# Kernel optimization log

Measured on AMD Instinct MI355X. Metric: run time of the kernel, lower is better.

Reference implementation:

```python
import jax, jax.numpy as jnp
import numpy as np

D = 768; NH = 12; DH = 64; DEPTH = 12; P = 16; IMG = 224; NC = 1000; DFF = 3072
GAMMA = 0.01; MIN_TOKENS = 16; EPS = 1e-6
SCALE = DH ** -0.5
NPATCH = (IMG // P) ** 2  # 196


def _ln(x, w, b, eps=1e-6):
    mu = x.mean(-1, keepdims=True)
    var = ((x - mu) ** 2).mean(-1, keepdims=True)
    return (x - mu) * jax.lax.rsqrt(var + eps) * w + b


def _block(x, p):
    # one pre-norm ViT block; returns new x, attention matrix A [B,H,T,T], values v [B,H,T,DH]
    (l1w, l1b, qw, qb, pw, pb, l2w, l2b, f1w, f1b, f2w, f2b) = p
    B, T, _ = x.shape
    qkv = _ln(x, l1w, l1b) @ qw + qb                      # [B,T,3D]
    qkv = qkv.reshape(B, T, 3, NH, DH).transpose(2, 0, 3, 1, 4)
    q, k, v = qkv[0], qkv[1], qkv[2]                      # [B,H,T,DH]
    A = jax.nn.softmax(jnp.einsum('bhtd,bhsd->bhts', q, k) * SCALE, axis=-1)
    out = jnp.einsum('bhts,bhsd->bhtd', A, v).transpose(0, 2, 1, 3).reshape(B, T, NH * DH)
    x = x + out @ pw + pb
    h = jax.nn.gelu(_ln(x, l2w, l2b) @ f1w + f1b, approximate=False)
    x = x + h @ f2w + f2b
    return x, A, v


def _embed(x, patch_w, patch_b, cls_token, pos_embed):
    B = x.shape[0]
    feat = jax.lax.conv_general_dilated(x, patch_w, (P, P), 'VALID',
                                        dimension_numbers=('NCHW', 'OIHW', 'NCHW'))  # [B,D,14,14]
    feat = feat.reshape(B, D, -1).transpose(0, 2, 1) + patch_b                       # [B,196,D]
    cls = jnp.broadcast_to(cls_token, (B, 1, D))
    return jnp.concatenate([cls, feat], axis=1) + pos_embed                          # [B,197,D]


def setup_inputs() -> dict:
    key = jax.random.key(0)
    ks = jax.random.split(key, 12)
    s = 0.02
    n = lambda k, shape: jax.random.normal(k, shape, jnp.float32) * s
    return {
        'x': jax.random.normal(ks[0], (32, 3, IMG, IMG), jnp.float32),
        'patch_w': n(ks[1], (D, 3, P, P)),
        'patch_b': jnp.zeros((D,), jnp.float32),
        'cls_token': n(ks[2], (1, 1, D)),
        'pos_embed': n(ks[3], (1, NPATCH + 1, D)),
        'ln1_w': jnp.ones((DEPTH, D), jnp.float32),
        'ln1_b': jnp.zeros((DEPTH, D), jnp.float32),
        'qkv_w': n(ks[4], (DEPTH, D, 3 * D)),
        'qkv_b': jnp.zeros((DEPTH, 3 * D), jnp.float32),
        'proj_w': n(ks[5], (DEPTH, D, D)),
        'proj_b': jnp.zeros((DEPTH, D), jnp.float32),
        'ln2_w': jnp.ones((DEPTH, D), jnp.float32),
        'ln2_b': jnp.zeros((DEPTH, D), jnp.float32),
        'fc1_w': n(ks[6], (DEPTH, D, DFF)),
        'fc1_b': jnp.zeros((DEPTH, DFF), jnp.float32),
        'fc2_w': n(ks[7], (DEPTH, DFF, D)),
        'fc2_b': jnp.zeros((DEPTH, D), jnp.float32),
        'norm_w': jnp.ones((D,), jnp.float32),
        'norm_b': jnp.zeros((D,), jnp.float32),
        'head_w': n(ks[8], (D, NC)),
        'head_b': jnp.zeros((NC,), jnp.float32),
    }


def reference(x, patch_w, patch_b, cls_token, pos_embed, ln1_w, ln1_b, qkv_w, qkv_b,
              proj_w, proj_b, ln2_w, ln2_b, fc1_w, fc1_b, fc2_w, fc2_b,
              norm_w, norm_b, head_w, head_b):
    # NOTE: token pruning produces data-dependent shapes, so this runs eagerly
    # (Python control flow on concrete values), exactly mirroring the torch code.
    x = _embed(x, patch_w, patch_b, cls_token, pos_embed)
    N = x.shape[1] - 1
    prev_mass = None
    for l in range(DEPTH):
        p = (ln1_w[l], ln1_b[l], qkv_w[l], qkv_b[l], proj_w[l], proj_b[l],
             ln2_w[l], ln2_b[l], fc1_w[l], fc1_b[l], fc2_w[l], fc2_b[l])
        x, A, v = _block(x, p)
        if N <= MIN_TOKENS:
            continue
        Am = A.mean(axis=1)                                   # [B,T,T] head-mean attention
        Vm = v.mean(axis=1)                                   # [B,T,DH] head-mean values
        rho = (1.0 + Am[:, 0, 0] * jnp.linalg.norm(Vm[:, 0], axis=-1)).mean()
        A_cls = Am[:, 0, 1:N + 1]                             # [B,N] cls->patch attention
        V_pt = Vm[:, 1:N + 1]
        Vc = V_pt - V_pt.mean(axis=1, keepdims=True)
        Vn = jnp.linalg.norm(Vc, axis=-1)                     # [B,N]
        mu = Vn.mean(axis=1, keepdims=True)
        sd = Vn.std(axis=1, keepdims=True, ddof=1)            # torch.std is unbiased
        J = A_cls * jax.nn.relu((Vn - mu) / (sd + EPS))       # [B,N] Jacobian score
        mass = J.sum(axis=1).mean()
        if prev_mass is not None:
            eta = mass / (prev_mass + EPS)
            keep_ratio = jnp.clip(rho * eta, 0.25, 4.0) ** (-GAMMA)
            N_next = max(MIN_TOKENS, int(N * float(keep_ratio)))
        else:
            N_next = N
        if N_next < N:
            idx = jnp.sort(jax.lax.top_k(J.mean(axis=0), N_next)[1]) + 1
            keep = jnp.concatenate([jnp.zeros((1,), idx.dtype), idx])
            x = x[:, keep]
            N = N_next
        prev_mass = mass
    x = _ln(x, norm_w, norm_b)
    return x[:, 0] @ head_w + head_b
```

## Files before the change

### kernel.cpp

```cpp
#include <hip/hip_runtime.h>
#include <math.h>

#define D 768
#define NH 12
#define DH 64
#define DEPTH 12
#define TMAX 197
#define NPATCH 196
#define BATCH 32
#define DFF 3072
#define NC 1000
#define QSTRIDE 2304
#define SCALE 0.125f
#define EPSF 1e-6f
#define MPAD 6400

typedef __bf16 bf16x8 __attribute__((ext_vector_type(8)));
typedef float f32x4 __attribute__((ext_vector_type(4)));
typedef short sshort8 __attribute__((ext_vector_type(8)));


__device__ __forceinline__ short f2bf(float x) {
  unsigned u = __float_as_uint(x);
  u = u + 0x7fffu + ((u >> 16) & 1u);
  return (short)(u >> 16);
}
__device__ __forceinline__ float bf2f(short h) {
  return __uint_as_float(((unsigned)(unsigned short)h) << 16);
}
__device__ __forceinline__ void bsplit(float x, short* hp, short* lp) {
  short h = f2bf(x);
  *hp = h;
  *lp = f2bf(x - bf2f(h));
}

__device__ __forceinline__ void gll16(const void* g, void* l) {
  __builtin_amdgcn_global_load_lds(
      (const __attribute__((address_space(1))) void*)g,
      (__attribute__((address_space(3))) void*)l, 16, 0, 0);
}


__device__ __forceinline__ float block_reduce_sum(float v, float* red, int tid) {
  red[tid] = v; __syncthreads();
  #pragma unroll
  for (int o = 128; o > 0; o >>= 1) { if (tid < o) red[tid] += red[tid + o]; __syncthreads(); }
  float r = red[0]; __syncthreads();
  return r;
}

__global__ void fail_kernel(float* out) { out[0] = 1.0e6f; }

__global__ void init_kernel(int* si, float* sf) {
  si[0] = TMAX;
  si[1] = 0;
  si[2] = 0;
  sf[0] = 0.f;
}

__global__ void wsplit_t(const float* __restrict__ W, short* __restrict__ Wpk,
                         int K, int N) {
  __shared__ float t[32][33];
  int n0 = blockIdx.x * 32, k0 = blockIdx.y * 32;
  int tid = threadIdx.x;
  int kk = tid >> 3, n4 = (tid & 7) * 4;
  float4 v = *(const float4*)(W + (size_t)(k0 + kk) * N + n0 + n4);
  t[kk][n4] = v.x; t[kk][n4 + 1] = v.y; t[kk][n4 + 2] = v.z; t[kk][n4 + 3] = v.w;
  __syncthreads();
  int nn = tid >> 3, k4 = (tid & 7) * 4;
  short* dh = Wpk + (size_t)(n0 + nn) * 2 * K + k0 + k4;
  short* dl = dh + K;
  #pragma unroll
  for (int c = 0; c < 4; ++c) bsplit(t[k4 + c][nn], &dh[c], &dl[c]);
}

__global__ void wsplit_nt(const float* __restrict__ W, short* __restrict__ Wpk, int K) {
  const float* src = W + (size_t)blockIdx.x * K;
  short* dh = Wpk + (size_t)blockIdx.x * 2 * K;
  short* dl = dh + K;
  for (int k = threadIdx.x; k < K; k += 256) bsplit(src[k], &dh[k], &dl[k]);
}


__global__ void im2col_kernel(const float* __restrict__ x, short* __restrict__ Impk) {
  int p = blockIdx.x, b = blockIdx.y;
  int py = p / 14, px = p % 14;
  short* dst = Impk + ((size_t)b * NPATCH + p) * 1536;
  for (int k = threadIdx.x; k < D; k += 256) {
    int c = k >> 8; int rem = k & 255; int i = rem >> 4; int j = rem & 15;
    float v = x[(((size_t)b * 3 + c) * 224 + py * 16 + i) * 224 + px * 16 + j];
    bsplit(v, &dst[k], &dst[768 + k]);
  }
}

__global__ void assemble_kernel(const float* __restrict__ PE, const float* __restrict__ cls,
                                const float* __restrict__ pos, float* __restrict__ X) {
  int t = blockIdx.x, b = blockIdx.y; int tid = threadIdx.x;
  float* xp = X + ((size_t)(b * TMAX) + t) * D;
  for (int k = tid; k < D; k += 256) {
    float v = (t == 0) ? cls[k] : PE[((size_t)(b * NPATCH) + (t - 1)) * D + k];
    xp[k] = v + pos[(size_t)t * D + k];
  }
}


__global__ void ln_kernel(const float* __restrict__ Xin, short* __restrict__ XNpk,
                          const float* __restrict__ wgt, const float* __restrict__ bsh,
                          const int* __restrict__ si) {
  int row = blockIdx.x;
  if ((row % TMAX) >= si[0]) return;
  __shared__ float red[256];
  int tid = threadIdx.x;
  const float* xp = Xin + (size_t)row * D;
  float v0 = xp[tid], v1 = xp[tid + 256], v2 = xp[tid + 512];
  float mu = block_reduce_sum(v0 + v1 + v2, red, tid) * (1.0f / 768.0f);
  float d0 = v0 - mu, d1 = v1 - mu, d2 = v2 - mu;
  float var = block_reduce_sum(d0 * d0 + d1 * d1 + d2 * d2, red, tid) * (1.0f / 768.0f);
  float inv = 1.0f / sqrtf(var + EPSF);
  short* op = XNpk + (size_t)row * 1536;
  float y0 = d0 * inv * wgt[tid] + bsh[tid];
  float y1 = d1 * inv * wgt[tid + 256] + bsh[tid + 256];
  float y2 = d2 * inv * wgt[tid + 512] + bsh[tid + 512];
  bsplit(y0, &op[tid], &op[768 + tid]);
  bsplit(y1, &op[tid + 256], &op[768 + tid + 256]);
  bsplit(y2, &op[tid + 512], &op[768 + tid + 512]);
}

__global__ void lnfinal_kernel(const float* __restrict__ X, float* __restrict__ CLSb,
                               const float* __restrict__ wgt, const float* __restrict__ bsh) {
  int b = blockIdx.x; int tid = threadIdx.x;
  __shared__ float red[256];
  const float* xp = X + (size_t)b * TMAX * D;
  float v0 = xp[tid], v1 = xp[tid + 256], v2 = xp[tid + 512];
  float mu = block_reduce_sum(v0 + v1 + v2, red, tid) * (1.0f / 768.0f);
  float d0 = v0 - mu, d1 = v1 - mu, d2 = v2 - mu;
  float var = block_reduce_sum(d0 * d0 + d1 * d1 + d2 * d2, red, tid) * (1.0f / 768.0f);
  float inv = 1.0f / sqrtf(var + EPSF);
  float* op = CLSb + (size_t)b * D;
  op[tid]       = d0 * inv * wgt[tid]       + bsh[tid];
  op[tid + 256] = d1 * inv * wgt[tid + 256] + bsh[tid + 256];
  op[tid + 512] = d2 * inv * wgt[tid + 512] + bsh[tid + 512];
}

__device__ __forceinline__ void swz_map(int d, int nx, int ny, int wsub,
                                        int& bx, int& by) {
  int q = ny >> 3, r = ny & 7;
  int rows, mb, l;
  int big = (q + 1) * nx;
  if (d < r * big) { int c = d / big; l = d - c * big; rows = q + 1; mb = c * (q + 1); }
  else { int d2 = d - r * big; int sm = q * nx; int c2 = d2 / sm; l = d2 - c2 * sm; rows = q; mb = r * (q + 1) + c2 * q; }
  int wspan = wsub * rows;
  int j = l / wspan; int t = l - j * wspan;
  int ml = t / wsub; int dx = t - ml * wsub;
  bx = j * wsub + dx; by = mb + ml;
}


#define GTM 128
#define GTN 128
#define GTK 32

template<int EPI, int SWZ>
__global__ __launch_bounds__(256)
void mgemm_kernel(const short* __restrict__ Apk, const short* __restrict__ Bpk,
                  const float* __restrict__ bias, const float* __restrict__ Rsrc,
                  float* __restrict__ Cf, short* __restrict__ Cpk,
                  int M, int K, int N, int nx, int ny, int wsub) {
  __shared__ char lds[65536];
  const int tid = threadIdx.x;
  const int ln = tid & 63;
  const int wv = tid >> 6;
  const int wm = wv >> 1, wn = wv & 1;

  int bx, by;
  if (SWZ) swz_map(blockIdx.x, nx, ny, wsub, bx, by);
  else { bx = blockIdx.x % nx; by = blockIdx.x / nx; }

  const int m0 = by * GTM, n0 = bx * GTN;
  const int lm = ln & 15, kc = ln >> 4;
  const size_t rs = 2 * (size_t)K;

  f32x4 acc[4][4];
  f32x4 zv = {0.f, 0.f, 0.f, 0.f};
  #pragma unroll
  for (int i = 0; i < 4; ++i)
    #pragma unroll
    for (int j = 0; j < 4; ++j) acc[i][j] = zv;

  auto stage = [&](int k0, int buf) {
    char* base = lds + (buf << 15);
    #pragma unroll
    for (int i = 0; i < 4; ++i) {
      int s = (i << 8) + tid;
      int r = s >> 3;
      int sl = (s & 7) ^ (r & 7);
      size_t eoff = (size_t)(sl >> 2) * K + (size_t)(k0 + ((sl & 3) << 3));
      int ldsoff = ((i << 8) + (tid & 192)) << 4;
      gll16(Apk + (size_t)(m0 + r) * rs + eoff, base + ldsoff);
      gll16(Bpk + (size_t)(n0 + r) * rs + eoff, base + 16384 + ldsoff);
    }
  };

  const int nk = K / GTK;
  stage(0, 0);
  for (int kt = 0; kt < nk; ++kt) {
    __syncthreads();
    if (kt + 1 < nk) stage((kt + 1) * GTK, (kt + 1) & 1);
    const char* pa = lds + ((kt & 1) << 15);
    const char* pb = pa + 16384;
    bf16x8 bh[4], bl[4];
    #pragma unroll
    for (int j = 0; j < 4; ++j) {
      int c = wn * 64 + j * 16 + lm;
      int bo = c * 128 + ((kc ^ (c & 7)) << 4);
      bh[j] = *(const bf16x8*)(pb + bo);
      bl[j] = *(const bf16x8*)(pb + (bo ^ 64));
    }
    #pragma unroll
    for (int i = 0; i < 4; ++i) {
      int r = wm * 64 + i * 16 + lm;
      int ao = r * 128 + ((kc ^ (r & 7)) << 4);
      bf16x8 ah = *(const bf16x8*)(pa + ao);
      bf16x8 al = *(const bf16x8*)(pa + (ao ^ 64));
      #pragma unroll
      for (int j = 0; j < 4; ++j) {
        acc[i][j] = __builtin_amdgcn_mfma_f32_16x16x32_bf16(ah, bh[j], acc[i][j], 0, 0, 0);
        acc[i][j] = __builtin_amdgcn_mfma_f32_16x16x32_bf16(ah, bl[j], acc[i][j], 0, 0, 0);
        acc[i][j] = __builtin_amdgcn_mfma_f32_16x16x32_bf16(al, bh[j], acc[i][j], 0, 0, 0);
      }
    }
  }

  #pragma unroll
  for (int i = 0; i < 4; ++i) {
    #pragma unroll
    for (int t = 0; t < 4; ++t) {
      int m = m0 + wm * 64 + i * 16 + kc * 4 + t;
      if (m >= M) continue;
      #pragma unroll
      for (int j = 0; j < 4; ++j) {
        int n = n0 + wn * 64 + j * 16 + lm;
        float v = acc[i][j][t] + bias[n];
        if (EPI == 1) v += Rsrc[(size_t)m * N + n];
        if (EPI == 2) {
          v = v * 0.5f * (1.0f + erff(v * 0.70710678118654752f));
          short h = f2bf(v);
          Cpk[(size_t)m * 2 * N + n] = h;
          Cpk[(size_t)m * 2 * N + N + n] = f2bf(v - bf2f(h));
        } else {
          Cf[(size_t)m * N + n] = v;
        }
      }
    }
  }
}


template<int EPI, int SWZ>
__global__ __launch_bounds__(512)
void mgemm256_kernel(const short* __restrict__ Apk, const short* __restrict__ Bpk,
                     const float* __restrict__ bias, const float* __restrict__ Rsrc,
                     float* __restrict__ Cf, short* __restrict__ Cpk,
                     int M, int K, int N, int nx, int ny, int wsub) {
  __shared__ char lds[131072];
  const int tid = threadIdx.x;
  const int ln = tid & 63;
  const int wv = tid >> 6;
  const int wm = wv >> 2, wn = wv & 3;

  int bx, by;
  if (SWZ) swz_map(blockIdx.x, nx, ny, wsub, bx, by);
  else { bx = blockIdx.x % nx; by = blockIdx.x / nx; }

  const int m0 = by * 256, n0 = bx * 256;
  const int lm = ln & 15, kc = ln >> 4;
  const size_t rs = 2 * (size_t)K;

  f32x4 acc[8][4];
  f32x4 zv = {0.f, 0.f, 0.f, 0.f};
  #pragma unroll
  for (int i = 0; i < 8; ++i)
    #pragma unroll
    for (int j = 0; j < 4; ++j) acc[i][j] = zv;

  auto stage = [&](int k0, int buf) {
    char* base = lds + (buf << 16);
    #pragma unroll
    for (int i = 0; i < 4; ++i) {
      int s = (i << 9) + tid;
      int r = s >> 3;
      int sl = (s & 7) ^ (r & 7);
      size_t eoff = (size_t)(sl >> 2) * K + (size_t)(k0 + ((sl & 3) << 3));
      int ldsoff = ((i << 9) + (tid & 448)) << 4;
      gll16(Apk + (size_t)(m0 + r) * rs + eoff, base + ldsoff);
      gll16(Bpk + (size_t)(n0 + r) * rs + eoff, base + 32768 + ldsoff);
    }
  };

  const int nk = K / GTK;
  stage(0, 0);
  for (int kt = 0; kt < nk; ++kt) {
    __syncthreads();
    if (kt + 1 < nk) stage((kt + 1) * GTK, (kt + 1) & 1);
    const char* pa = lds + ((kt & 1) << 16);
    const char* pb = pa + 32768;
    bf16x8 bh[4], bl[4];
    #pragma unroll
    for (int j = 0; j < 4; ++j) {
      int c = wn * 64 + j * 16 + lm;
      int bo = c * 128 + ((kc ^ (c & 7)) << 4);
      bh[j] = *(const bf16x8*)(pb + bo);
      bl[j] = *(const bf16x8*)(pb + (bo ^ 64));
    }
    #pragma unroll
    for (int i = 0; i < 8; ++i) {
      int r = wm * 128 + i * 16 + lm;
      int ao = r * 128 + ((kc ^ (r & 7)) << 4);
      bf16x8 ah = *(const bf16x8*)(pa + ao);
      bf16x8 al = *(const bf16x8*)(pa + (ao ^ 64));
      #pragma unroll
      for (int j = 0; j < 4; ++j) {
        acc[i][j] = __builtin_amdgcn_mfma_f32_16x16x32_bf16(ah, bh[j], acc[i][j], 0, 0, 0);
        acc[i][j] = __builtin_amdgcn_mfma_f32_16x16x32_bf16(ah, bl[j], acc[i][j], 0, 0, 0);
        acc[i][j] = __builtin_amdgcn_mfma_f32_16x16x32_bf16(al, bh[j], acc[i][j], 0, 0, 0);
      }
    }
  }

  #pragma unroll
  for (int i = 0; i < 8; ++i) {
    #pragma unroll
    for (int t = 0; t < 4; ++t) {
      int m = m0 + wm * 128 + i * 16 + kc * 4 + t;
      if (m >= M) continue;
      #pragma unroll
      for (int j = 0; j < 4; ++j) {
        int n = n0 + wn * 64 + j * 16 + lm;
        float v = acc[i][j][t] + bias[n];
        if (EPI == 1) v += Rsrc[(size_t)m * N + n];
        if (EPI == 2) {
          v = v * 0.5f * (1.0f + erff(v * 0.70710678118654752f));
          short h = f2bf(v);
          Cpk[(size_t)m * 2 * N + n] = h;
          Cpk[(size_t)m * 2 * N + N + n] = f2bf(v - bf2f(h));
        } else {
          Cf[(size_t)m * N + n] = v;
        }
      }
    }
  }
}


#define BM 128
#define BN 64
#define BK 16

__global__ __launch_bounds__(256, 2)
void gemm_kernel(const float* __restrict__ A, const float* __restrict__ Bw,
                 const float* __restrict__ bias, float* __restrict__ C,
                 int M, int K, int N) {
  __shared__ float As[BK][BM + 4];
  __shared__ float Bs[BK][BN];
  int tid = threadIdx.x;
  int tx = tid & 15;
  int ty = tid >> 4;
  int m0 = blockIdx.y * BM;
  int n0 = blockIdx.x * BN;
  float acc[8][4];
  #pragma unroll
  for (int i = 0; i < 8; ++i)
    #pragma unroll
    for (int j = 0; j < 4; ++j) acc[i][j] = 0.f;
  const int lkA = tid & 15;
  const int lmA = tid >> 4;
  const int lnB = tid & 63;
  const int lkB = tid >> 6;
  for (int k0 = 0; k0 < K; k0 += BK) {
    #pragma unroll
    for (int r = 0; r < 8; ++r) {
      int ml = r * 16 + lmA;
      int m = m0 + ml;
      float va = 0.f;
      if (m < M) va = A[(size_t)m * K + k0 + lkA];
      As[lkA][ml] = va;
    }
    #pragma unroll
    for (int r = 0; r < 4; ++r) {
      int kk = r * 4 + lkB;
      int n = n0 + lnB;
      float vb = 0.f;
      if (n < N) vb = Bw[(size_t)(k0 + kk) * N + n];
      Bs[kk][lnB] = vb;
    }
    __syncthreads();
    #pragma unroll
    for (int kk = 0; kk < BK; ++kk) {
      const float4 b4 = *(const float4*)(&Bs[kk][tx * 4]);
      const float4 a0 = *(const float4*)(&As[kk][ty * 8]);
      const float4 a1 = *(const float4*)(&As[kk][ty * 8 + 4]);
      const float a[8] = {a0.x, a0.y, a0.z, a0.w, a1.x, a1.y, a1.z, a1.w};
      const float bb[4] = {b4.x, b4.y, b4.z, b4.w};
      #pragma unroll
      for (int i = 0; i < 8; ++i)
        #pragma unroll
        for (int j = 0; j < 4; ++j)
          acc[i][j] = fmaf(a[i], bb[j], acc[i][j]);
    }
    __syncthreads();
  }
  #pragma unroll
  for (int i = 0; i < 8; ++i) {
    int m = m0 + ty * 8 + i;
    if (m >= M) continue;
    #pragma unroll
    for (int j = 0; j < 4; ++j) {
      int n = n0 + tx * 4 + j;
      if (n >= N) continue;
      C[(size_t)m * N + n] = acc[i][j] + bias[n];
    }
  }
}


#define QT 64
#define KVT 64

__global__ __launch_bounds__(256)
void mattn_kernel(const float* __restrict__ QKV, short* __restrict__ AOpk,
                  const int* __restrict__ si) {
  const int tok = si[0];
  const int bh = blockIdx.x; const int b = bh / NH, h = bh % NH;
  const int q0 = blockIdx.y * QT;
  if (q0 >= tok) return;
  __shared__ short Kh[4096], Kl[4096], Vth[4096], Vtl[4096];
  __shared__ short Pb[8192];
  const int tid = threadIdx.x;
  const int l = tid & 63, w = tid >> 6;
  const int lm = l & 15, lg = l >> 4;

  bf16x8 qh[2], ql[2];
  {
    int qrow = q0 + w * 16 + lm;
    if (qrow >= TMAX) qrow = TMAX - 1;
    const float* qp = QKV + (size_t)(b * TMAX + qrow) * QSTRIDE + h * DH + lg * 8;
    #pragma unroll
    for (int c = 0; c < 2; ++c) {
      sshort8 hs, ls;
      #pragma unroll
      for (int j = 0; j < 8; ++j) {
        float v = qp[c * 32 + j];
        short hh = f2bf(v);
        hs[j] = hh;
        ls[j] = f2bf(v - bf2f(hh));
      }
      qh[c] = __builtin_bit_cast(bf16x8, hs);
      ql[c] = __builtin_bit_cast(bf16x8, ls);
    }
  }

  float mrun[4], lrun[4];
  f32x4 oacc[4];
  f32x4 zv = {0.f, 0.f, 0.f, 0.f};
  #pragma unroll
  for (int t = 0; t < 4; ++t) { mrun[t] = -1e30f; lrun[t] = 0.f; }
  #pragma unroll
  for (int j = 0; j < 4; ++j) oacc[j] = zv;

  const int r0 = (tid >> 4) * 4;
  const int td4 = (tid & 15) * 4;

  for (int j0 = 0; j0 < tok; j0 += KVT) {
    {
      float vbuf[16];
      #pragma unroll
      for (int i = 0; i < 4; ++i) {
        int gr = j0 + r0 + i; if (gr >= TMAX) gr = TMAX - 1;
        const float* kp = QKV + (size_t)(b * TMAX + gr) * QSTRIDE + D + h * DH + td4;
        float4 kv = *(const float4*)kp;
        short4 sh, sl;
        sh.x = f2bf(kv.x); sl.x = f2bf(kv.x - bf2f(sh.x));
        sh.y = f2bf(kv.y); sl.y = f2bf(kv.y - bf2f(sh.y));
        sh.z = f2bf(kv.z); sl.z = f2bf(kv.z - bf2f(sh.z));
        sh.w = f2bf(kv.w); sl.w = f2bf(kv.w - bf2f(sh.w));
        int r = r0 + i;
        int so = r * 64 + (((td4 >> 3) ^ (r & 7)) << 3) + (td4 & 7);
        *(short4*)(Kh + so) = sh;
        *(short4*)(Kl + so) = sl;
        const float* vp = QKV + (size_t)(b * TMAX + gr) * QSTRIDE + 2 * D + h * DH + td4;
        float4 vv = *(const float4*)vp;
        vbuf[i * 4 + 0] = vv.x; vbuf[i * 4 + 1] = vv.y;
        vbuf[i * 4 + 2] = vv.z; vbuf[i * 4 + 3] = vv.w;
      }
      #pragma unroll
      for (int dd = 0; dd < 4; ++dd) {
        int d = td4 + dd;
        short4 sh, sl;
        float c0 = vbuf[dd], c1 = vbuf[4 + dd], c2 = vbuf[8 + dd], c3 = vbuf[12 + dd];
        sh.x = f2bf(c0); sl.x = f2bf(c0 - bf2f(sh.x));
        sh.y = f2bf(c1); sl.y = f2bf(c1 - bf2f(sh.y));
        sh.z = f2bf(c2); sl.z = f2bf(c2 - bf2f(sh.z));
        sh.w = f2bf(c3); sl.w = f2bf(c3 - bf2f(sh.w));
        int so = d * 64 + (((r0 >> 3) ^ (d & 7)) << 3) + (r0 & 7);
        *(short4*)(Vth + so) = sh;
        *(short4*)(Vtl + so) = sl;
      }
    }
    __syncthreads();

    f32x4 sacc[4];
    #pragma unroll
    for (int jk = 0; jk < 4; ++jk) sacc[jk] = zv;
    #pragma unroll
    for (int c = 0; c < 2; ++c) {
      #pragma unroll
      for (int jk = 0; jk < 4; ++jk) {
        int row = jk * 16 + lm;
        int so = row * 64 + (((c * 4 + lg) ^ (row & 7)) << 3);
        bf16x8 kbh = *(const bf16x8*)(Kh + so);
        bf16x8 kbl = *(const bf16x8*)(Kl + so);
        sacc[jk] = __builtin_amdgcn_mfma_f32_16x16x32_bf16(qh[c], kbh, sacc[jk], 0, 0, 0);
        sacc[jk] = __builtin_amdgcn_mfma_f32_16x16x32_bf16(qh[c], kbl, sacc[jk], 0, 0, 0);
        sacc[jk] = __builtin_amdgcn_mfma_f32_16x16x32_bf16(ql[c], kbh, sacc[jk], 0, 0, 0);
      }
    }

    float p[4][4];
    #pragma unroll
    for (int jk = 0; jk < 4; ++jk) {
      bool valid = (j0 + jk * 16 + lm) < tok;
      #pragma unroll
      for (int t = 0; t < 4; ++t)
        p[jk][t] = valid ? sacc[jk][t] * SCALE : -1e30f;
    }
    float mt[4], mnew[4], co[4], rsm[4];
    #pragma unroll
    for (int t = 0; t < 4; ++t) {
      mt[t] = fmaxf(fmaxf(p[0][t], p[1][t]), fmaxf(p[2][t], p[3][t]));
      #pragma unroll
      for (int off = 1; off < 16; off <<= 1)
        mt[t] = fmaxf(mt[t], __shfl_xor(mt[t], off, 16));
      mnew[t] = fmaxf(mrun[t], mt[t]);
      co[t] = expf(mrun[t] - mnew[t]);
      rsm[t] = 0.f;
    }
    #pragma unroll
    for (int jk = 0; jk < 4; ++jk)
      #pragma unroll
      for (int t = 0; t < 4; ++t) {
        p[jk][t] = expf(p[jk][t] - mnew[t]);
        rsm[t] += p[jk][t];
      }
    #pragma unroll
    for (int t = 0; t < 4; ++t) {
      #pragma unroll
      for (int off = 1; off < 16; off <<= 1)
        rsm[t] += __shfl_xor(rsm[t], off, 16);
      lrun[t] = lrun[t] * co[t] + rsm[t];
      mrun[t] = mnew[t];
    }
    #pragma unroll
    for (int jd = 0; jd < 4; ++jd)
      #pragma unroll
      for (int t = 0; t < 4; ++t) oacc[jd][t] *= co[t];

    short* Pw = Pb + w * 2048;
    #pragma unroll
    for (int jk = 0; jk < 4; ++jk)
      #pragma unroll
      for (int t = 0; t < 4; ++t) {
        int q = lg * 4 + t;
        int col = jk * 16 + lm;
        short hh = f2bf(p[jk][t]);
        short hl = f2bf(p[jk][t] - bf2f(hh));
        int so = q * 64 + (((col >> 3) ^ (q & 7)) << 3) + (col & 7);
        Pw[so] = hh;
        Pw[1024 + so] = hl;
      }

    #pragma unroll
    for (int c = 0; c < 2; ++c) {
      int aro = lm * 64 + (((c * 4 + lg) ^ (lm & 7)) << 3);
      bf16x8 pah = *(const bf16x8*)(Pw + aro);
      bf16x8 pal = *(const bf16x8*)(Pw + 1024 + aro);
      #pragma unroll
      for (int jd = 0; jd < 4; ++jd) {
        int d = jd * 16 + lm;
        int so = d * 64 + (((c * 4 + lg) ^ (d & 7)) << 3);
        bf16x8 vbh = *(const bf16x8*)(Vth + so);
        bf16x8 vbl = *(const bf16x8*)(Vtl + so);
        oacc[jd] = __builtin_amdgcn_mfma_f32_16x16x32_bf16(pah, vbh, oacc[jd], 0, 0, 0);
        oacc[jd] = __builtin_amdgcn_mfma_f32_16x16x32_bf16(pah, vbl, oacc[jd], 0, 0, 0);
        oacc[jd] = __builtin_amdgcn_mfma_f32_16x16x32_bf16(pal, vbh, oacc[jd], 0, 0, 0);
      }
    }
    __syncthreads();
  }

  #pragma unroll
  for (int t = 0; t < 4; ++t) {
    int q = q0 + w * 16 + lg * 4 + t;
    if (q >= tok) continue;
    float inv = 1.0f / lrun[t];
    short* op = AOpk + (size_t)(b * TMAX + q) * 1536 + h * DH;
    #pragma unroll
    for (int jd = 0; jd < 4; ++jd) {
      int d = jd * 16 + lm;
      float y = oacc[jd][t] * inv;
      short hh = f2bf(y);
      op[d] = hh;
      op[768 + d] = f2bf(y - bf2f(hh));
    }
  }
}

__global__ void clsrow_kernel(const float* __restrict__ QKV, float* __restrict__ Pcls,
                              const int* __restrict__ si) {
  int tok = si[0];
  int bh = blockIdx.x; int b = bh / NH, h = bh % NH;
  int tid = threadIdx.x;
  __shared__ float q[DH];
  __shared__ float red[256];
  if (tid < DH) q[tid] = QKV[((size_t)(b * TMAX)) * QSTRIDE + h * DH + tid];
  __syncthreads();
  float sval = -1e30f;
  if (tid < tok) {
    const float* kp = QKV + ((size_t)(b * TMAX) + tid) * QSTRIDE + D + h * DH;
    float a = 0.f;
    #pragma unroll
    for (int dd = 0; dd < DH; ++dd) a = fmaf(q[dd], kp[dd], a);
    sval = a * SCALE;
  }
  red[tid] = sval; __syncthreads();
  #pragma unroll
  for (int o = 128; o > 0; o >>= 1) { if (tid < o) red[tid] = fmaxf(red[tid], red[tid + o]); __syncthreads(); }
  float mx = red[0]; __syncthreads();
  float e = (tid < tok) ? expf(sval - mx) : 0.f;
  red[tid] = e; __syncthreads();
  #pragma unroll
  for (int o = 128; o > 0; o >>= 1) { if (tid < o) red[tid] += red[tid + o]; __syncthreads(); }
  if (tid < tok) Pcls[(size_t)bh * TMAX + tid] = e / red[0];
}

__global__ void aclsmean_kernel(const float* __restrict__ Pcls, float* __restrict__ Acls,
                                const int* __restrict__ si) {
  int tok = si[0]; int b = blockIdx.x; int tid = threadIdx.x;
  if (tid < tok) {
    float s = 0.f;
    #pragma unroll
    for (int h = 0; h < NH; ++h) s += Pcls[((size_t)b * NH + h) * TMAX + tid];
    Acls[b * TMAX + tid] = s * (1.0f / 12.0f);
  }
}

__global__ void vmean_kernel(const float* __restrict__ QKV, float* __restrict__ Vm,
                             const int* __restrict__ si) {
  int tok = si[0];
  int t = blockIdx.x, b = blockIdx.y;
  if (t >= tok) return;
  int d = threadIdx.x;
  const float* vp = QKV + ((size_t)(b * TMAX + t)) * QSTRIDE + 2 * D;
  float s = 0.f;
  #pragma unroll
  for (int h = 0; h < NH; ++h) s += vp[h * DH + d];
  Vm[((size_t)b * TMAX + t) * DH + d] = s * (1.0f / 12.0f);
}


__global__ void stats_kernel(const float* __restrict__ Vm, const float* __restrict__ Acls,
                             float* __restrict__ Jbuf, float* __restrict__ Jsum,
                             float* __restrict__ rhot, const int* __restrict__ si) {
  int tok = si[0]; int N = tok - 1;
  if (N <= 16) return;
  int b = blockIdx.x; int tid = threadIdx.x;
  __shared__ float red[256];
  __shared__ float vmean[DH];
  __shared__ float Vn[NPATCH];
  const float* vb = Vm + (size_t)b * TMAX * DH;

  float x0 = 0.f;
  if (tid < DH) { float v = vb[tid]; x0 = v * v; }
  red[tid] = x0; __syncthreads();
  #pragma unroll
  for (int o = 128; o > 0; o >>= 1) { if (tid < o) red[tid] += red[tid + o]; __syncthreads(); }
  if (tid == 0) rhot[b] = 1.0f + Acls[b * TMAX] * sqrtf(red[0]);
  __syncthreads();

  int d = tid & 63, part = tid >> 6;
  float s = 0.f;
  for (int t = 1 + part; t <= N; t += 4) s += vb[(size_t)t * DH + d];
  red[tid] = s; __syncthreads();
  if (tid < DH) vmean[tid] = (red[tid] + red[tid + 64] + red[tid + 128] + red[tid + 192]) / (float)N;
  __syncthreads();

  if (tid < N) {
    const float* vp = vb + (size_t)(tid + 1) * DH;
    float a = 0.f;
    #pragma unroll
    for (int dd = 0; dd < DH; ++dd) { float z = vp[dd] - vmean[dd]; a = fmaf(z, z, a); }
    Vn[tid] = sqrtf(a);
  }
  __syncthreads();

  red[tid] = (tid < N) ? Vn[tid] : 0.f; __syncthreads();
  #pragma unroll
  for (int o = 128; o > 0; o >>= 1) { if (tid < o) red[tid] += red[tid + o]; __syncthreads(); }
  float mu = red[0] / (float)N;
  __syncthreads();
  float dv = (tid < N) ? (Vn[tid] - mu) : 0.f;
  red[tid] = dv * dv; __syncthreads();
  #pragma unroll
  for (int o = 128; o > 0; o >>= 1) { if (tid < o) red[tid] += red[tid + o]; __syncthreads(); }
  float sd = sqrtf(red[0] / (float)(N - 1));
  __syncthreads();

  float Jv = 0.f;
  if (tid < N) {
    float z = (Vn[tid] - mu) / (sd + EPSF);
    z = fmaxf(z, 0.f);
    Jv = Acls[b * TMAX + 1 + tid] * z;
    Jbuf[b * NPATCH + tid] = Jv;
  }
  red[tid] = Jv; __syncthreads();
  #pragma unroll
  for (int o = 128; o > 0; o >>= 1) { if (tid < o) red[tid] += red[tid + o]; __syncthreads(); }
  if (tid == 0) Jsum[b] = red[0];
}

__global__ void decide_kernel(const float* __restrict__ Jbuf, const float* __restrict__ Jsum,
                              const float* __restrict__ rhot, int* __restrict__ keep,
                              int* __restrict__ si, float* __restrict__ sf) {
  int tok = si[0]; int N = tok - 1;
  int tid = threadIdx.x;
  if (N <= 16) { if (tid == 0) si[2] = 0; return; }
  __shared__ float red[256];
  __shared__ float Jms[NPATCH];
  __shared__ int sel[NPATCH];

  red[tid] = (tid < BATCH) ? rhot[tid] : 0.f; __syncthreads();
  #pragma unroll
  for (int o = 128; o > 0; o >>= 1) { if (tid < o) red[tid] += red[tid + o]; __syncthreads(); }
  float rho = red[0] / (float)BATCH; __syncthreads();
  red[tid] = (tid < BATCH) ? Jsum[tid] : 0.f; __syncthreads();
  #pragma unroll
  for (int o = 128; o > 0; o >>= 1) { if (tid < o) red[tid] += red[tid + o]; __syncthreads(); }
  float mass = red[0] / (float)BATCH;
  int prev_valid = si[1];
  float prev = sf[0];
  __syncthreads();

  int N_next = N;
  if (prev_valid) {
    float eta = mass / (prev + EPSF);
    float re = rho * eta;
    re = fminf(fmaxf(re, 0.25f), 4.0f);
    double kr = pow((double)re, -0.01);
    int nn = (int)((double)N * kr);
    N_next = nn > 16 ? nn : 16;
  }
  if (tid == 0) { si[1] = 1; sf[0] = mass; }

  if (N_next < N) {
    if (tid < N) {
      float sJ = 0.f;
      for (int bb = 0; bb < BATCH; ++bb) sJ += Jbuf[bb * NPATCH + tid];
      Jms[tid] = sJ / (float)BATCH;
    }
    __syncthreads();
    if (tid < N) {
      float me = Jms[tid]; int rank = 0;
      for (int s2 = 0; s2 < N; ++s2) {
        float ov = Jms[s2];
        if (ov > me || (ov == me && s2 < tid)) ++rank;
      }
      sel[tid] = (rank < N_next) ? 1 : 0;
    }
    __syncthreads();
    if (tid == 0) {
      int c = 0; keep[c++] = 0;
      for (int t2 = 0; t2 < N; ++t2) if (sel[t2]) keep[c++] = t2 + 1;
      si[0] = N_next + 1;
      si[2] = 1;
    }
  } else {
    if (tid == 0) si[2] = 0;
  }
}

__global__ void gather_kernel(const float* __restrict__ X, float* __restrict__ T,
                              const int* __restrict__ keep, const int* __restrict__ si) {
  if (!si[2]) return;
  int tok = si[0];
  int i = blockIdx.x, b = blockIdx.y;
  if (i >= tok) return;
  int src = keep[i];
  const float* xp = X + ((size_t)(b * TMAX) + src) * D;
  float* tp = T + ((size_t)(b * TMAX) + i) * D;
  int tid = threadIdx.x;
  tp[tid] = xp[tid]; tp[tid + 256] = xp[tid + 256]; tp[tid + 512] = xp[tid + 512];
}

__global__ void copyback_kernel(const float* __restrict__ T, float* __restrict__ X,
                                const int* __restrict__ si) {
  if (!si[2]) return;
  int tok = si[0];
  int i = blockIdx.x, b = blockIdx.y;
  if (i >= tok) return;
  const float* tp = T + ((size_t)(b * TMAX) + i) * D;
  float* xp = X + ((size_t)(b * TMAX) + i) * D;
  int tid = threadIdx.x;
  xp[tid] = tp[tid]; xp[tid + 256] = tp[tid + 256]; xp[tid + 512] = tp[tid + 512];
}


extern "C" void kernel_launch(void* const* d_in, const int* in_sizes, int n_in,
                              void* d_out, int out_size, void* d_ws, size_t ws_size,
                              hipStream_t stream) {
  (void)in_sizes; (void)n_in; (void)out_size;
  const float* x       = (const float*)d_in[0];
  const float* patch_w = (const float*)d_in[1];
  const float* patch_b = (const float*)d_in[2];
  const float* cls_tok = (const float*)d_in[3];
  const float* pos     = (const float*)d_in[4];
  const float* ln1w    = (const float*)d_in[5];
  const float* ln1b    = (const float*)d_in[6];
  const float* qkvw    = (const float*)d_in[7];
  const float* qkvb    = (const float*)d_in[8];
  const float* projw   = (const float*)d_in[9];
  const float* projb   = (const float*)d_in[10];
  const float* ln2w    = (const float*)d_in[11];
  const float* ln2b    = (const float*)d_in[12];
  const float* fc1w    = (const float*)d_in[13];
  const float* fc1b    = (const float*)d_in[14];
  const float* fc2w    = (const float*)d_in[15];
  const float* fc2b    = (const float*)d_in[16];
  const float* normw   = (const float*)d_in[17];
  const float* normb   = (const float*)d_in[18];
  const float* headw   = (const float*)d_in[19];
  const float* headb   = (const float*)d_in[20];
  float* out = (float*)d_out;

  char* w = (char*)d_ws;
  size_t off = 0;
  auto alloc = [&](size_t bytes) -> void* {
    void* p = w + off;
    off += (bytes + 255) & ~(size_t)255;
    return p;
  };
  const size_t MROWS = (size_t)BATCH * TMAX;
  float* X    = (float*)alloc(MROWS * D * 4);
  short* XNpk = (short*)alloc((size_t)MPAD * 1536 * 2);
  float* QKV  = (float*)alloc(MROWS * QSTRIDE * 4);
  short* AOpk = (short*)alloc((size_t)MPAD * 1536 * 2);
  short* Hpk  = (short*)alloc((size_t)MPAD * 2 * DFF * 2);
  float* Vm   = (float*)alloc(MROWS * DH * 4);
  float* Pcls = (float*)alloc((size_t)BATCH * NH * TMAX * 4);
  float* Acls = (float*)alloc((size_t)BATCH * TMAX * 4);
  float* Jbuf = (float*)alloc((size_t)BATCH * NPATCH * 4);
  float* Jsum = (float*)alloc(BATCH * 4);
  float* rhot = (float*)alloc(BATCH * 4);
  int*   keep = (int*)alloc(256 * 4);
  int*   si   = (int*)alloc(64 * 4);
  float* sf   = (float*)alloc(64 * 4);
  float* CLS  = (float*)alloc((size_t)BATCH * D * 4);
  short* Wq   = (short*)alloc((size_t)QSTRIDE * 2 * D * 2);
  short* Wp   = (short*)alloc((size_t)D * 2 * D * 2);
  short* W1   = (short*)alloc((size_t)DFF * 2 * D * 2);
  short* W2   = (short*)alloc((size_t)D * 2 * DFF * 2);
  short* Wpat = (short*)alloc((size_t)D * 2 * D * 2);
  short* Impk = Hpk;
  float* TMP  = (float*)Hpk;
  float* Ef32 = QKV;

  if (off > ws_size) {
    fail_kernel<<<1, 1, 0, stream>>>(out);
    return;
  }

  init_kernel<<<1, 1, 0, stream>>>(si, sf);

  im2col_kernel<<<dim3(NPATCH, BATCH), 256, 0, stream>>>(x, Impk);
  wsplit_nt<<<D, 256, 0, stream>>>(patch_w, Wpat, D);
  mgemm_kernel<0, 1><<<6 * 49, 256, 0, stream>>>(
      Impk, Wpat, patch_b, nullptr, Ef32, nullptr, BATCH * NPATCH, D, D, 6, 49, 6);
  assemble_kernel<<<dim3(TMAX, BATCH), 256, 0, stream>>>(Ef32, cls_tok, pos, X);

  for (int l = 0; l < DEPTH; ++l) {
    const float* l1w = ln1w + l * D;
    const float* l1b = ln1b + l * D;
    const float* qw  = qkvw + (size_t)l * D * 3 * D;
    const float* qb  = qkvb + (size_t)l * 3 * D;
    const float* pw  = projw + (size_t)l * D * D;
    const float* pb  = projb + (size_t)l * D;
    const float* l2w = ln2w + l * D;
    const float* l2b = ln2b + l * D;
    const float* f1w = fc1w + (size_t)l * D * DFF;
    const float* f1b = fc1b + (size_t)l * DFF;
    const float* f2w = fc2w + (size_t)l * DFF * D;
    const float* f2b = fc2b + (size_t)l * D;

    wsplit_t<<<dim3(QSTRIDE / 32, D / 32), 256, 0, stream>>>(qw, Wq, D, QSTRIDE);
    wsplit_t<<<dim3(D / 32, D / 32), 256, 0, stream>>>(pw, Wp, D, D);
    wsplit_t<<<dim3(DFF / 32, D / 32), 256, 0, stream>>>(f1w, W1, D, DFF);
    wsplit_t<<<dim3(D / 32, DFF / 32), 256, 0, stream>>>(f2w, W2, DFF, D);

    ln_kernel<<<BATCH * TMAX, 256, 0, stream>>>(X, XNpk, l1w, l1b, si);
    mgemm256_kernel<0, 1><<<9 * 25, 512, 0, stream>>>(
        XNpk, Wq, qb, nullptr, QKV, nullptr, (int)MROWS, D, QSTRIDE, 9, 25, 3);
    mattn_kernel<<<dim3(BATCH * NH, (TMAX + QT - 1) / QT), 256, 0, stream>>>(QKV, AOpk, si);
    clsrow_kernel<<<BATCH * NH, 256, 0, stream>>>(QKV, Pcls, si);
    aclsmean_kernel<<<BATCH, 256, 0, stream>>>(Pcls, Acls, si);
    vmean_kernel<<<dim3(TMAX, BATCH), 64, 0, stream>>>(QKV, Vm, si);
    mgemm_kernel<1, 1><<<6 * 50, 256, 0, stream>>>(
        AOpk, Wp, pb, X, X, nullptr, (int)MROWS, D, D, 6, 50, 6);
    ln_kernel<<<BATCH * TMAX, 256, 0, stream>>>(X, XNpk, l2w, l2b, si);
    mgemm256_kernel<2, 1><<<12 * 25, 512, 0, stream>>>(
        XNpk, W1, f1b, nullptr, nullptr, Hpk, (int)MROWS, D, DFF, 12, 25, 4);
    mgemm_kernel<1, 0><<<6 * 50, 256, 0, stream>>>(
        Hpk, W2, f2b, X, X, nullptr, (int)MROWS, DFF, D, 6, 50, 6);
    stats_kernel<<<BATCH, 256, 0, stream>>>(Vm, Acls, Jbuf, Jsum, rhot, si);
    decide_kernel<<<1, 256, 0, stream>>>(Jbuf, Jsum, rhot, keep, si, sf);
    gather_kernel<<<dim3(TMAX, BATCH), 256, 0, stream>>>(X, TMP, keep, si);
    copyback_kernel<<<dim3(TMAX, BATCH), 256, 0, stream>>>(TMP, X, si);
  }

  lnfinal_kernel<<<BATCH, 256, 0, stream>>>(X, CLS, normw, normb);
  gemm_kernel<<<dim3(16, 1), 256, 0, stream>>>(CLS, headw, headb, out, BATCH, D, NC);
}
```

Baseline: 6.783 ms.

## Split 256-tile GEMM k-loop into four phases interleaving prefetch with MFMA

Restructures the 256x256 bf16x3 GEMM main loop into four phases, each reading two A sub-tiles from LDS and issuing MFMAs at raised wave priority. The next tile's A and B global-to-LDS loads are spread across the first two phases, with explicit barriers, waitcnts and sched_barriers replacing the single __syncthreads. The goal is to overlap global prefetch and LDS reads with matrix-core work in a ping-pong style schedule. In exchange it adds more barriers per k-step and relies on hand-placed waitcnts for correctness.

```diff
diff --git a/kernel.cpp b/kernel.cpp
--- a/kernel.cpp
+++ b/kernel.cpp
@@ -256,12 +256,31 @@
 }
 
 
+#define MFMA3(ACC, AH, AL, BH, BL) \
+  ACC = __builtin_amdgcn_mfma_f32_16x16x32_bf16(AH, BH, ACC, 0, 0, 0); \
+  ACC = __builtin_amdgcn_mfma_f32_16x16x32_bf16(AH, BL, ACC, 0, 0, 0); \
+  ACC = __builtin_amdgcn_mfma_f32_16x16x32_bf16(AL, BH, ACC, 0, 0, 0);
+
+#define READ_A(I, AH, AL) \
+  { int r_ = wm * 128 + (I) * 16 + lm; int ao_ = r_ * 128 + ((kc ^ (r_ & 7)) << 4); \
+    AH = *(const bf16x8*)(pa + ao_); AL = *(const bf16x8*)(pa + (ao_ ^ 64)); }
+
+#define PHASE_MID() \
+  __builtin_amdgcn_s_barrier(); \
+  asm volatile("s_waitcnt lgkmcnt(0)" ::: "memory"); \
+  __builtin_amdgcn_sched_barrier(0); \
+  __builtin_amdgcn_s_setprio(1);
+
+#define PHASE_END() \
+  __builtin_amdgcn_s_setprio(0); \
+  __builtin_amdgcn_s_barrier();
+
 template<int EPI, int SWZ>
 __global__ __launch_bounds__(512)
-void mgemm256_kernel(const short* __restrict__ Apk, const short* __restrict__ Bpk,
-                     const float* __restrict__ bias, const float* __restrict__ Rsrc,
-                     float* __restrict__ Cf, short* __restrict__ Cpk,
-                     int M, int K, int N, int nx, int ny, int wsub) {
+void mgemm256p_kernel(const short* __restrict__ Apk, const short* __restrict__ Bpk,
+                      const float* __restrict__ bias, const float* __restrict__ Rsrc,
+                      float* __restrict__ Cf, short* __restrict__ Cpk,
+                      int M, int K, int N, int nx, int ny, int wsub) {
   __shared__ char lds[131072];
   const int tid = threadIdx.x;
   const int ln = tid & 63;
@@ -283,7 +302,7 @@
     #pragma unroll
     for (int j = 0; j < 4; ++j) acc[i][j] = zv;
 
-  auto stage = [&](int k0, int buf) {
+  auto stageA = [&](int k0, int buf) {
     char* base = lds + (buf << 16);
     #pragma unroll
     for (int i = 0; i < 4; ++i) {
@@ -293,37 +312,95 @@
       size_t eoff = (size_t)(sl >> 2) * K + (size_t)(k0 + ((sl & 3) << 3));
       int ldsoff = ((i << 9) + (tid & 448)) << 4;
       gll16(Apk + (size_t)(m0 + r) * rs + eoff, base + ldsoff);
-      gll16(Bpk + (size_t)(n0 + r) * rs + eoff, base + 32768 + ldsoff);
     }
   };
+  auto stageB = [&](int k0, int buf) {
+    char* base = lds + (buf << 16) + 32768;
+    #pragma unroll
+    for (int i = 0; i < 4; ++i) {
+      int s = (i << 9) + tid;
+      int r = s >> 3;
+      int sl = (s & 7) ^ (r & 7);
+      size_t eoff = (size_t)(sl >> 2) * K + (size_t)(k0 + ((sl & 3) << 3));
+      int ldsoff = ((i << 9) + (tid & 448)) << 4;
+      gll16(Bpk + (size_t)(n0 + r) * rs + eoff, base + ldsoff);
+    }
+  };
 
   const int nk = K / GTK;
-  stage(0, 0);
+  stageA(0, 0);
+  stageB(0, 0);
+  asm volatile("s_waitcnt vmcnt(0)" ::: "memory");
+  __builtin_amdgcn_s_barrier();
+  __builtin_amdgcn_sched_barrier(0);
+
   for (int kt = 0; kt < nk; ++kt) {
-    __syncthreads();
-    if (kt + 1 < nk) stage((kt + 1) * GTK, (kt + 1) & 1);
-    const char* pa = lds + ((kt & 1) << 16);
+    const int cur = kt & 1;
+    const char* pa = lds + (cur << 16);
     const char* pb = pa + 32768;
+    const bool pf = (kt + 1 < nk);
+    const int knext = (kt + 1) * GTK;
     bf16x8 bh[4], bl[4];
-    #pragma unroll
-    for (int j = 0; j < 4; ++j) {
-      int c = wn * 64 + j * 16 + lm;
-      int bo = c * 128 + ((kc ^ (c & 7)) << 4);
-      bh[j] = *(const bf16x8*)(pb + bo);
-      bl[j] = *(const bf16x8*)(pb + (bo ^ 64));
-    }
-    #pragma unroll
-    for (int i = 0; i < 8; ++i) {
-      int r = wm * 128 + i * 16 + lm;
-      int ao = r * 128 + ((kc ^ (r & 7)) << 4);
-      bf16x8 ah = *(const bf16x8*)(pa + ao);
-      bf16x8 al = *(const bf16x8*)(pa + (ao ^ 64));
+
+    {
       #pragma unroll
       for (int j = 0; j < 4; ++j) {
-        acc[i][j] = __builtin_amdgcn_mfma_f32_16x16x32_bf16(ah, bh[j], acc[i][j], 0, 0, 0);
-        acc[i][j] = __builtin_amdgcn_mfma_f32_16x16x32_bf16(ah, bl[j], acc[i][j], 0, 0, 0);
-        acc[i][j] = __builtin_amdgcn_mfma_f32_16x16x32_bf16(al, bh[j], acc[i][j], 0, 0, 0);
-      }
+        int c = wn * 64 + j * 16 + lm;
+        int bo = c * 128 + ((kc ^ (c & 7)) << 4);
+        bh[j] = *(const bf16x8*)(pb + bo);
+        bl[j] = *(const bf16x8*)(pb + (bo ^ 64));
+      }
+      bf16x8 ah0, al0, ah1, al1;
+      READ_A(0, ah0, al0);
+      READ_A(1, ah1, al1);
+      if (pf) stageA(knext, cur ^ 1);
+      PHASE_MID();
+      #pragma unroll
+      for (int j = 0; j < 4; ++j) {
+        MFMA3(acc[0][j], ah0, al0, bh[j], bl[j]);
+        MFMA3(acc[1][j], ah1, al1, bh[j], bl[j]);
+      }
+      PHASE_END();
+    }
+    {
+      bf16x8 ah0, al0, ah1, al1;
+      READ_A(2, ah0, al0);
+      READ_A(3, ah1, al1);
+      if (pf) stageB(knext, cur ^ 1);
+      PHASE_MID();
+      #pragma unroll
+      for (int j = 0; j < 4; ++j) {
+        MFMA3(acc[2][j], ah0, al0, bh[j], bl[j]);
+        MFMA3(acc[3][j], ah1, al1, bh[j], bl[j]);
+      }
+      PHASE_END();
+    }
+    {
+      bf16x8 ah0, al0, ah1, al1;
+      READ_A(4, ah0, al0);
+      READ_A(5, ah1, al1);
+      PHASE_MID();
+      #pragma unroll
+      for (int j = 0; j < 4; ++j) {
+        MFMA3(acc[4][j], ah0, al0, bh[j], bl[j]);
+        MFMA3(acc[5][j], ah1, al1, bh[j], bl[j]);
+      }
+      PHASE_END();
+    }
+    {
+      bf16x8 ah0, al0, ah1, al1;
+      READ_A(6, ah0, al0);
+      READ_A(7, ah1, al1);
+      PHASE_MID();
+      #pragma unroll
+      for (int j = 0; j < 4; ++j) {
+        MFMA3(acc[6][j], ah0, al0, bh[j], bl[j]);
+        MFMA3(acc[7][j], ah1, al1, bh[j], bl[j]);
+      }
+      __builtin_amdgcn_s_setprio(0);
+      asm volatile("s_waitcnt vmcnt(0)" ::: "memory");
+      __builtin_amdgcn_s_barrier();
+      __builtin_amdgcn_sched_barrier(0);
     }
   }
 
@@ -905,7 +982,7 @@
     wsplit_t<<<dim3(D / 32, DFF / 32), 256, 0, stream>>>(f2w, W2, DFF, D);
 
     ln_kernel<<<BATCH * TMAX, 256, 0, stream>>>(X, XNpk, l1w, l1b, si);
-    mgemm256_kernel<0, 1><<<9 * 25, 512, 0, stream>>>(
+    mgemm256p_kernel<0, 1><<<9 * 25, 512, 0, stream>>>(
         XNpk, Wq, qb, nullptr, QKV, nullptr, (int)MROWS, D, QSTRIDE, 9, 25, 3);
     mattn_kernel<<<dim3(BATCH * NH, (TMAX + QT - 1) / QT), 256, 0, stream>>>(QKV, AOpk, si);
     clsrow_kernel<<<BATCH * NH, 256, 0, stream>>>(QKV, Pcls, si);
@@ -914,7 +991,7 @@
     mgemm_kernel<1, 1><<<6 * 50, 256, 0, stream>>>(
         AOpk, Wp, pb, X, X, nullptr, (int)MROWS, D, D, 6, 50, 6);
     ln_kernel<<<BATCH * TMAX, 256, 0, stream>>>(X, XNpk, l2w, l2b, si);
-    mgemm256_kernel<2, 1><<<12 * 25, 512, 0, stream>>>(
+    mgemm256p_kernel<2, 1><<<12 * 25, 512, 0, stream>>>(
         XNpk, W1, f1b, nullptr, nullptr, Hpk, (int)MROWS, D, DFF, 12, 25, 4);
     mgemm_kernel<1, 0><<<6 * 50, 256, 0, stream>>>(
         Hpk, W2, f2b, X, X, nullptr, (int)MROWS, DFF, D, 6, 50, 6);
```

New measurement: 6.943 ms. 2.4% more time.
